# Kernel tuning notes

Measured on AMD Instinct MI355X. Metric: run time of the kernel, lower is better.

## Reference

```python
import jax, jax.numpy as jnp
import numpy as np

B, N, D, H, L, ML, NS = 2, 512, 256, 8, 4, 512, 1000
DH = D // H
DFF = 4 * D

def _layer_norm(x, g, b, eps=1e-5):
    m = jnp.mean(x, -1, keepdims=True)
    v = jnp.var(x, -1, keepdims=True)
    return (x - m) / jnp.sqrt(v + eps) * g + b

def _safe_norm(sq):
    # torch.norm has zero subgradient at 0 (diagonal of pairwise diffs)
    pos = sq > 0
    return jnp.where(pos, jnp.sqrt(jnp.where(pos, sq, 1.0)), 0.0)

def setup_inputs() -> dict:
    key = jax.random.key(0)
    ks = iter(jax.random.split(key, 64))
    w = lambda shape: jax.random.normal(next(ks), shape, jnp.float32) * 0.05
    inp = {
        'x': jax.random.normal(next(ks), (B, N, 3), jnp.float32),
        't': jax.random.randint(next(ks), (B,), 0, NS),
        'mask': jnp.ones((B, N), bool),
        'W_time': w((D, 1)), 'b_time': jnp.zeros((D,), jnp.float32),
        'W_in': w((D, 3 + D)), 'b_in': jnp.zeros((D,), jnp.float32),
        'rel_pos': jax.random.normal(next(ks), (2 * ML - 1, D), jnp.float32),
        'qkv_W': w((L, 3 * D, D)), 'qkv_b': jnp.zeros((L, 3 * D), jnp.float32),
        'ao_W': w((L, D, D)), 'ao_b': jnp.zeros((L, D), jnp.float32),
        'geo_W': w((L, H, 2)), 'geo_b': jnp.zeros((L, H), jnp.float32),
        'pos_W': w((L, H, D)), 'pos_b': jnp.zeros((L, H), jnp.float32),
        'ln1_g': jnp.ones((L, D), jnp.float32), 'ln1_b': jnp.zeros((L, D), jnp.float32),
        'ln2_g': jnp.ones((L, D), jnp.float32), 'ln2_b': jnp.zeros((L, D), jnp.float32),
        'fc1_W': w((L, DFF, D)), 'fc1_b': jnp.zeros((L, DFF), jnp.float32),
        'fc2_W': w((L, D, DFF)), 'fc2_b': jnp.zeros((L, D), jnp.float32),
        'W_out': w((3, D)), 'b_out': jnp.zeros((3,), jnp.float32),
    }
    return inp

def _forward(x, t, mask, W_time, b_time, W_in, b_in, rel_pos, qkv_W, qkv_b, ao_W, ao_b,
             geo_W, geo_b, pos_W, pos_b, ln1_g, ln1_b, ln2_g, ln2_b,
             fc1_W, fc1_b, fc2_W, fc2_b, W_out, b_out):
    tf = (t.astype(jnp.float32) / NS)[:, None]                      # (B,1)
    t_embed = jax.nn.relu(tf @ W_time.T + b_time)[:, None, :]       # (B,1,D)
    t_embed = jnp.broadcast_to(t_embed, (B, N, D))
    h = jax.nn.relu(jnp.concatenate([x, t_embed], -1) @ W_in.T + b_in)  # (B,N,D)

    pos_idx = jnp.arange(N)[:, None] - jnp.arange(N)[None, :] + (ML - 1)
    pe = rel_pos[pos_idx]                                           # (N,N,D)
    mask_j = mask[:, None, None, :]                                 # (B,1,1,N)

    for l in range(L):
        # geometric features: pairwise distance + diag of diff@diff^T (= squared dist)
        diff = h[:, :, None, :] - h[:, None, :, :]                  # (B,N,N,D)
        sq = jnp.sum(diff * diff, -1)                               # (B,N,N)
        geo = jnp.stack([_safe_norm(sq), sq], -1)                   # (B,N,N,2)
        geo_w = jnp.einsum('bijc,hc->bhij', geo, geo_W[l]) + geo_b[l][None, :, None, None]
        pos_w = jnp.einsum('ijd,hd->hij', pe, pos_W[l]) + pos_b[l][:, None, None]

        qkv = (h @ qkv_W[l].T + qkv_b[l]).reshape(B, N, 3, H, DH)
        q, k, v = qkv[:, :, 0], qkv[:, :, 1], qkv[:, :, 2]          # (B,N,H,DH)
        logits = jnp.einsum('bihd,bjhd->bhij', q, k) / np.sqrt(DH)
        logits = logits + geo_w + pos_w[None]
        logits = jnp.where(mask_j, logits, -jnp.inf)
        attn = jax.nn.softmax(logits, -1)
        ao = jnp.einsum('bhij,bjhd->bihd', attn, v).reshape(B, N, D)
        ao = ao @ ao_W[l].T + ao_b[l]

        h = _layer_norm(h + ao, ln1_g[l], ln1_b[l])
        ffn = jax.nn.relu(h @ fc1_W[l].T + fc1_b[l]) @ fc2_W[l].T + fc2_b[l]
        ffn = ffn * mask[:, :, None]
        h = _layer_norm(h + ffn, ln2_g[l], ln2_b[l])

    out = h @ W_out.T + b_out
    return out * mask[:, :, None]

def reference(x, t, mask, W_time, b_time, W_in, b_in, rel_pos, qkv_W, qkv_b, ao_W, ao_b,
              geo_W, geo_b, pos_W, pos_b, ln1_g, ln1_b, ln2_g, ln2_b,
              fc1_W, fc1_b, fc2_W, fc2_b, W_out, b_out):
    return _forward(x, t, mask, W_time, b_time, W_in, b_in, rel_pos, qkv_W, qkv_b,
                    ao_W, ao_b, geo_W, geo_b, pos_W, pos_b, ln1_g, ln1_b, ln2_g, ln2_b,
                    fc1_W, fc1_b, fc2_W, fc2_b, W_out, b_out)
```

## Files before the change

### kernel.cpp

```cpp
#include <hip/hip_runtime.h>
#include <hip/hip_bf16.h>
#include <math.h>


#define B_ 2
#define N_ 512
#define D_ 256
#define H_ 8
#define L_ 4
#define ROWS_ (B_ * N_)

typedef __bf16 bf16;
typedef __bf16 b16x8 __attribute__((ext_vector_type(8)));
typedef __bf16 b16x4 __attribute__((ext_vector_type(4)));
typedef float  f32x4 __attribute__((ext_vector_type(4)));

__global__ void u_kernel(const int* __restrict__ t, const float* __restrict__ W_time,
                         const float* __restrict__ b_time, const float* __restrict__ W_in,
                         const float* __restrict__ b_in, float* __restrict__ u)
{
    int b = blockIdx.x, tid = threadIdx.x;
    __shared__ float te[D_];
    float tf = (float)t[b] / 1000.0f;
    te[tid] = fmaxf(tf * W_time[tid] + b_time[tid], 0.0f);
    __syncthreads();
    float acc = b_in[tid];
    const float* wrow = W_in + (size_t)tid * 259 + 3;
    #pragma unroll 4
    for (int k = 0; k < D_; ++k) acc += wrow[k] * te[k];
    u[b * D_ + tid] = acc;
}

__global__ __launch_bounds__(256) void h0bf_kernel(
    const float* __restrict__ x, const float* __restrict__ W_in,
    const float* __restrict__ u, float* __restrict__ h,
    bf16* __restrict__ hb, float* __restrict__ r2)
{
    int w = threadIdx.x >> 6, lane = threadIdx.x & 63;
    int row = blockIdx.x * 4 + w;
    int b = row >> 9;
    float x0 = x[row * 3 + 0], x1 = x[row * 3 + 1], x2 = x[row * 3 + 2];
    float vv[4];
    #pragma unroll
    for (int e = 0; e < 4; ++e) {
        int d = lane * 4 + e;
        const float* wr = W_in + (size_t)d * 259;
        vv[e] = fmaxf(wr[0] * x0 + wr[1] * x1 + wr[2] * x2 + u[b * D_ + d], 0.0f);
    }
    float4 v = make_float4(vv[0], vv[1], vv[2], vv[3]);
    ((float4*)(h + (size_t)row * D_))[lane] = v;
    b16x4 rb = {(bf16)v.x, (bf16)v.y, (bf16)v.z, (bf16)v.w};
    ((b16x4*)(hb + (size_t)row * D_))[lane] = rb;
    float bx = (float)rb[0], by = (float)rb[1], bz = (float)rb[2], bw = (float)rb[3];
    float q2 = bx * bx + by * by + bz * bz + bw * bw;
    #pragma unroll
    for (int o = 1; o < 64; o <<= 1) q2 += __shfl_xor(q2, o);
    if (lane == 0) r2[row] = q2;
}

__global__ void wcvt_all(const float* __restrict__ qW, const float* __restrict__ aW,
                         const float* __restrict__ f1W, const float* __restrict__ f2W,
                         bf16* __restrict__ dst)
{
    size_t idx = ((size_t)blockIdx.x * 256 + threadIdx.x) * 4;
    int l = (int)(idx / 786432);
    int rem = (int)(idx % 786432);
    const float* src; size_t off;
    if (rem < 196608)      { src = qW  + (size_t)l * 196608; off = rem; }
    else if (rem < 262144) { src = aW  + (size_t)l * 65536;  off = rem - 196608; }
    else if (rem < 524288) { src = f1W + (size_t)l * 262144; off = rem - 262144; }
    else                   { src = f2W + (size_t)l * 262144; off = rem - 524288; }
    float4 v = *(const float4*)(src + off);
    b16x4 r = {(bf16)v.x, (bf16)v.y, (bf16)v.z, (bf16)v.w};
    *(b16x4*)(dst + idx) = r;
}

__global__ void posr_kernel(const float* __restrict__ rel_pos, const float* __restrict__ pos_W,
                            const float* __restrict__ pos_b, float* __restrict__ posr)
{
    int p = blockIdx.x, tid = threadIdx.x;
    __shared__ float pe[D_];
    pe[tid] = rel_pos[(size_t)p * D_ + tid];
    __syncthreads();
    if (tid < L_ * H_) {
        const float* w = pos_W + (size_t)tid * D_;
        float acc = pos_b[tid];
        #pragma unroll 4
        for (int d = 0; d < D_; ++d) acc += pe[d] * w[d];
        posr[(size_t)tid * 1023 + p] = acc;
    }
}

__global__ __launch_bounds__(256) void gemm_bf16(
    const bf16* __restrict__ A, const bf16* __restrict__ W,
    const float* __restrict__ bias, float* __restrict__ Cf, bf16* __restrict__ Cb,
    int M, int Nout, int K, int relu)
{
    __shared__ __align__(16) bf16 As[64 * 64];
    __shared__ __align__(16) bf16 Bs[64 * 64];
    const int tid = threadIdx.x;
    const int bn = blockIdx.x * 64, bm = blockIdx.y * 64;
    const int lane = tid & 63, w = tid >> 6;
    const int wr = w >> 1, wc = w & 1;
    const int r15 = lane & 15, kg = lane >> 4;

    f32x4 acc[2][2] = {};

    const int srow = tid >> 2, q = tid & 3;
    for (int k0 = 0; k0 < K; k0 += 64) {
        const bf16* sa = A + (size_t)(bm + srow) * K + k0 + q * 16;
        b16x8 a0 = *(const b16x8*)sa, a1 = *(const b16x8*)(sa + 8);
        *(b16x8*)&As[srow * 64 + (((2 * q) ^ (srow & 7)) << 3)] = a0;
        *(b16x8*)&As[srow * 64 + (((2 * q + 1) ^ (srow & 7)) << 3)] = a1;
        const bf16* sb = W + (size_t)(bn + srow) * K + k0 + q * 16;
        b16x8 b0 = *(const b16x8*)sb, b1 = *(const b16x8*)(sb + 8);
        *(b16x8*)&Bs[srow * 64 + (((2 * q) ^ (srow & 7)) << 3)] = b0;
        *(b16x8*)&Bs[srow * 64 + (((2 * q + 1) ^ (srow & 7)) << 3)] = b1;
        __syncthreads();

        #pragma unroll
        for (int kt = 0; kt < 2; ++kt) {
            int kc = kt * 4 + kg;
            b16x8 av[2], bv[2];
            #pragma unroll
            for (int f = 0; f < 2; ++f) {
                int ar = wr * 32 + f * 16 + r15;
                av[f] = *(const b16x8*)&As[ar * 64 + ((kc ^ (ar & 7)) << 3)];
                int br = wc * 32 + f * 16 + r15;
                bv[f] = *(const b16x8*)&Bs[br * 64 + ((kc ^ (br & 7)) << 3)];
            }
            acc[0][0] = __builtin_amdgcn_mfma_f32_16x16x32_bf16(av[0], bv[0], acc[0][0], 0, 0, 0);
            acc[0][1] = __builtin_amdgcn_mfma_f32_16x16x32_bf16(av[0], bv[1], acc[0][1], 0, 0, 0);
            acc[1][0] = __builtin_amdgcn_mfma_f32_16x16x32_bf16(av[1], bv[0], acc[1][0], 0, 0, 0);
            acc[1][1] = __builtin_amdgcn_mfma_f32_16x16x32_bf16(av[1], bv[1], acc[1][1], 0, 0, 0);
        }
        __syncthreads();
    }

    const int r4 = lane >> 4;
    #pragma unroll
    for (int fm = 0; fm < 2; ++fm) {
        #pragma unroll
        for (int fn = 0; fn < 2; ++fn) {
            int col = bn + wc * 32 + fn * 16 + r15;
            float bc = bias[col];
            #pragma unroll
            for (int r = 0; r < 4; ++r) {
                int rowi = bm + wr * 32 + fm * 16 + r4 * 4 + r;
                float v = acc[fm][fn][r] + bc;
                if (relu) v = fmaxf(v, 0.0f);
                if (Cb) Cb[(size_t)rowi * Nout + col] = (bf16)v;
                else    Cf[(size_t)rowi * Nout + col] = v;
            }
        }
    }
}

__global__ __launch_bounds__(256) void fatgemm_kernel(
    const bf16* __restrict__ hb, const bf16* __restrict__ Wq,
    const float* __restrict__ qB, bf16* __restrict__ qkd, bf16* __restrict__ vt,
    const float* __restrict__ r2, float* __restrict__ sq)
{
    __shared__ __align__(16) bf16 As[64 * 64];
    __shared__ __align__(16) bf16 Bs[64 * 64];
    const int tid = threadIdx.x;
    const int lane = tid & 63, w = tid >> 6;
    const int wr = w >> 1, wc = w & 1;
    const int r15 = lane & 15, kg = lane >> 4;

    const bool isq = blockIdx.x < 192;
    int bn, bm, gb = 0;
    const bf16 *Ap, *Bp;
    if (isq) {
        bn = (blockIdx.x % 12) * 64; bm = (blockIdx.x / 12) * 64;
        Ap = hb + (size_t)bm * 256;  Bp = Wq + (size_t)bn * 256;
    } else {
        int idx = blockIdx.x - 192;
        gb = idx >> 6;
        int i2 = idx & 63;
        bn = (i2 & 7) * 64;
        bm = (i2 >> 3) * 64;
        Ap = hb + ((size_t)gb * 512 + bm) * 256;
        Bp = hb + ((size_t)gb * 512 + bn) * 256;
    }

    f32x4 acc[2][2] = {};
    const int srow = tid >> 2, q = tid & 3;
    for (int k0 = 0; k0 < 256; k0 += 64) {
        const bf16* sa = Ap + (size_t)srow * 256 + k0 + q * 16;
        b16x8 a0 = *(const b16x8*)sa, a1 = *(const b16x8*)(sa + 8);
        *(b16x8*)&As[srow * 64 + (((2 * q) ^ (srow & 7)) << 3)] = a0;
        *(b16x8*)&As[srow * 64 + (((2 * q + 1) ^ (srow & 7)) << 3)] = a1;
        const bf16* sb = Bp + (size_t)srow * 256 + k0 + q * 16;
        b16x8 b0 = *(const b16x8*)sb, b1 = *(const b16x8*)(sb + 8);
        *(b16x8*)&Bs[srow * 64 + (((2 * q) ^ (srow & 7)) << 3)] = b0;
        *(b16x8*)&Bs[srow * 64 + (((2 * q + 1) ^ (srow & 7)) << 3)] = b1;
        __syncthreads();

        #pragma unroll
        for (int kt = 0; kt < 2; ++kt) {
            int kc = kt * 4 + kg;
            b16x8 av[2], bv[2];
            #pragma unroll
            for (int f = 0; f < 2; ++f) {
                int ar = wr * 32 + f * 16 + r15;
                av[f] = *(const b16x8*)&As[ar * 64 + ((kc ^ (ar & 7)) << 3)];
                int br = wc * 32 + f * 16 + r15;
                bv[f] = *(const b16x8*)&Bs[br * 64 + ((kc ^ (br & 7)) << 3)];
            }
            acc[0][0] = __builtin_amdgcn_mfma_f32_16x16x32_bf16(av[0], bv[0], acc[0][0], 0, 0, 0);
            acc[0][1] = __builtin_amdgcn_mfma_f32_16x16x32_bf16(av[0], bv[1], acc[0][1], 0, 0, 0);
            acc[1][0] = __builtin_amdgcn_mfma_f32_16x16x32_bf16(av[1], bv[0], acc[1][0], 0, 0, 0);
            acc[1][1] = __builtin_amdgcn_mfma_f32_16x16x32_bf16(av[1], bv[1], acc[1][1], 0, 0, 0);
        }
        __syncthreads();
    }

    const int r4 = lane >> 4;
    if (isq) {
        #pragma unroll
        for (int fm = 0; fm < 2; ++fm) {
            #pragma unroll
            for (int fn = 0; fn < 2; ++fn) {
                int col = bn + wc * 32 + fn * 16 + r15;
                float bc = qB[col];
                #pragma unroll
                for (int r = 0; r < 4; ++r) {
                    int rowi = bm + wr * 32 + fm * 16 + r4 * 4 + r;
                    float v = acc[fm][fn][r] + bc;
                    if (col < 512) {
                        qkd[(size_t)rowi * 512 + col] = (bf16)v;
                    } else {
                        int hd = col - 512, hhh = hd >> 5, d = hd & 31;
                        int bb = rowi >> 9, j = rowi & 511;
                        vt[(((size_t)bb * 8 + hhh) * 32 + d) * 512 + j] = (bf16)v;
                    }
                }
            }
        }
    } else {
        const float* r2b = r2 + gb * 512;
        #pragma unroll
        for (int fm = 0; fm < 2; ++fm) {
            #pragma unroll
            for (int fn = 0; fn < 2; ++fn) {
                int j = bn + wc * 32 + fn * 16 + r15;
                float r2j = r2b[j];
                #pragma unroll
                for (int r = 0; r < 4; ++r) {
                    int i = bm + wr * 32 + fm * 16 + r4 * 4 + r;
                    sq[((size_t)gb * 512 + i) * 512 + j] = r2b[i] + r2j - 2.0f * acc[fm][fn][r];
                }
            }
        }
    }
}

__global__ __launch_bounds__(256) void attn_mfma(
    const bf16* __restrict__ qk,
    const bf16* __restrict__ vt,
    const float* __restrict__ sq, const float* __restrict__ posr,
    const float* __restrict__ geoW, const float* __restrict__ geoB,
    bf16* __restrict__ ao)
{
    __shared__ __align__(16) bf16 p_lds[4][2048];
    __shared__ float pos_lds[528];
    __shared__ float olds[4 * 528];
    __shared__ float maxs[4][16];
    __shared__ float sums[4][16];

    const int tid = threadIdx.x;
    const int w = tid >> 6, lane = tid & 63;
    const int qt = blockIdx.x, hh = blockIdx.y, b = blockIdx.z;
    const int q0 = qt * 16;
    const int r15 = lane & 15, kg = lane >> 4;
    const int j0w = w * 128;

    for (int i = tid; i < 527; i += 256) pos_lds[i] = posr[hh * 1023 + q0 + i];
    __syncthreads();

    b16x8 qf = *(const b16x8*)(qk + ((size_t)(b * 512 + q0 + r15)) * 512 + hh * 32 + kg * 8);

    f32x4 zero = {};
    f32x4 st[8];
    #pragma unroll
    for (int jt = 0; jt < 8; ++jt) {
        b16x8 kf = *(const b16x8*)(qk + ((size_t)(b * 512 + j0w + jt * 16 + r15)) * 512
                                      + 256 + hh * 32 + kg * 8);
        st[jt] = __builtin_amdgcn_mfma_f32_16x16x32_bf16(kf, qf, zero, 0, 0, 0);
    }

    const float gw0 = geoW[hh * 2], gw1 = geoW[hh * 2 + 1], gb = geoB[hh];
    const float inv = 0.17677669529663687f;
    const int qq = q0 + r15;
    const float* sqrow = sq + ((size_t)b * 512 + qq) * 512;

    #pragma unroll
    for (int jt = 0; jt < 8; ++jt) {
        int jb = j0w + jt * 16 + kg * 4;
        float4 s4 = *(const float4*)(sqrow + jb);
        #pragma unroll
        for (int r = 0; r < 4; ++r) {
            float sv = (r == 0) ? s4.x : (r == 1) ? s4.y : (r == 2) ? s4.z : s4.w;
            float sn = sv > 0.0f ? sqrtf(sv) : 0.0f;
            st[jt][r] = st[jt][r] * inv + gw0 * sn + gw1 * sv + gb
                      + pos_lds[r15 - (jb + r) + 511];
        }
    }

    float mx = -3e38f;
    #pragma unroll
    for (int jt = 0; jt < 8; ++jt) {
        #pragma unroll
        for (int r = 0; r < 4; ++r) mx = fmaxf(mx, st[jt][r]);
    }
    mx = fmaxf(mx, __shfl_xor(mx, 16));
    mx = fmaxf(mx, __shfl_xor(mx, 32));
    if (lane < 16) maxs[w][r15] = mx;
    __syncthreads();
    float M = fmaxf(fmaxf(maxs[0][r15], maxs[1][r15]), fmaxf(maxs[2][r15], maxs[3][r15]));
    float sm = 0.0f;
    #pragma unroll
    for (int jt = 0; jt < 8; ++jt) {
        #pragma unroll
        for (int r = 0; r < 4; ++r) {
            float e = __expf(st[jt][r] - M);
            st[jt][r] = e; sm += e;
        }
    }
    sm += __shfl_xor(sm, 16);
    sm += __shfl_xor(sm, 32);
    if (lane < 16) sums[w][r15] = sm;

    #pragma unroll
    for (int jt = 0; jt < 8; ++jt) {
        int cc = jt * 2 + (kg >> 1);
        int ccs = cc ^ (r15 & 7);
        b16x4 p4 = {(bf16)st[jt][0], (bf16)st[jt][1], (bf16)st[jt][2], (bf16)st[jt][3]};
        *(b16x4*)&p_lds[w][r15 * 128 + ccs * 8 + (kg & 1) * 4] = p4;
    }

    f32x4 oacc[2] = {};
    #pragma unroll
    for (int jc = 0; jc < 4; ++jc) {
        int ccs = (jc * 4 + kg) ^ (r15 & 7);
        b16x8 pf = *(const b16x8*)&p_lds[w][r15 * 128 + ccs * 8];
        #pragma unroll
        for (int dt = 0; dt < 2; ++dt) {
            b16x8 vf = *(const b16x8*)(vt + (((size_t)(b * 8 + hh)) * 32 + dt * 16 + r15) * 512
                                          + j0w + jc * 32 + kg * 8);
            oacc[dt] = __builtin_amdgcn_mfma_f32_16x16x32_bf16(pf, vf, oacc[dt], 0, 0, 0);
        }
    }
    #pragma unroll
    for (int dt = 0; dt < 2; ++dt) {
        #pragma unroll
        for (int r = 0; r < 4; ++r)
            olds[w * 528 + (kg * 4 + r) * 33 + dt * 16 + r15] = oacc[dt][r];
    }
    __syncthreads();

    #pragma unroll
    for (int it = 0; it < 2; ++it) {
        int idx = tid + it * 256;
        int row = idx >> 5, d = idx & 31;
        float T = sums[0][row] + sums[1][row] + sums[2][row] + sums[3][row];
        float val = olds[row * 33 + d] + olds[528 + row * 33 + d]
                  + olds[1056 + row * 33 + d] + olds[1584 + row * 33 + d];
        ao[((size_t)(b * 512 + q0 + row)) * 256 + hh * 32 + d] = (bf16)(val / T);
    }
}

template <int K>
__global__ __launch_bounds__(256) void gemmln_kernel(
    const bf16* __restrict__ A, const bf16* __restrict__ W,
    const float* __restrict__ bias, float* __restrict__ h,
    const float* __restrict__ g, const float* __restrict__ beta,
    bf16* __restrict__ hb, float* __restrict__ r2out)
{
    __shared__ __align__(16) bf16 As[16 * K];
    __shared__ float reds[3][4][16];
    const int tid = threadIdx.x;
    const int row0 = blockIdx.x * 16;
    const int lane = tid & 63, w = tid >> 6;
    const int r15 = lane & 15, kg = lane >> 4;
    constexpr int NCH = K / 8;
    constexpr int CPT = (16 * NCH) / 256;

    #pragma unroll
    for (int e = 0; e < CPT; ++e) {
        int gch = tid * CPT + e;
        int row = gch / NCH, c = gch % NCH;
        int slab = c >> 3, c3 = c & 7;
        b16x8 v = *(const b16x8*)(A + (size_t)(row0 + row) * K + c * 8);
        *(b16x8*)&As[slab * 1024 + row * 64 + ((c3 ^ (row & 7)) << 3)] = v;
    }
    __syncthreads();

    f32x4 acc[4] = {};
    #pragma unroll 4
    for (int kt = 0; kt < K / 32; ++kt) {
        int slab = kt >> 1, kc2 = (kt & 1) * 4 + kg;
        b16x8 af = *(const b16x8*)&As[slab * 1024 + r15 * 64 + ((kc2 ^ (r15 & 7)) << 3)];
        #pragma unroll
        for (int t = 0; t < 4; ++t) {
            int col = w * 64 + t * 16 + r15;
            b16x8 bf = *(const b16x8*)(W + (size_t)col * K + kt * 32 + kg * 8);
            acc[t] = __builtin_amdgcn_mfma_f32_16x16x32_bf16(af, bf, acc[t], 0, 0, 0);
        }
    }

    float val[4][4];
    #pragma unroll
    for (int t = 0; t < 4; ++t) {
        int col = w * 64 + t * 16 + r15;
        float bc = bias[col];
        #pragma unroll
        for (int r = 0; r < 4; ++r)
            val[t][r] = acc[t][r] + bc + h[(size_t)(row0 + kg * 4 + r) * 256 + col];
    }

    float s[4];
    #pragma unroll
    for (int r = 0; r < 4; ++r) {
        s[r] = val[0][r] + val[1][r] + val[2][r] + val[3][r];
        #pragma unroll
        for (int o = 1; o < 16; o <<= 1) s[r] += __shfl_xor(s[r], o);
    }
    if (r15 == 0) {
        for (int r = 0; r < 4; ++r) reds[0][w][kg * 4 + r] = s[r];
    }
    __syncthreads();
    float mean[4];
    #pragma unroll
    for (int r = 0; r < 4; ++r) {
        int row = kg * 4 + r;
        mean[r] = (reds[0][0][row] + reds[0][1][row] + reds[0][2][row] + reds[0][3][row]) * (1.0f / 256.0f);
    }
    #pragma unroll
    for (int r = 0; r < 4; ++r) {
        float q = 0.0f;
        #pragma unroll
        for (int t = 0; t < 4; ++t) { float d = val[t][r] - mean[r]; q += d * d; }
        #pragma unroll
        for (int o = 1; o < 16; o <<= 1) q += __shfl_xor(q, o);
        s[r] = q;
    }
    __syncthreads();
    if (r15 == 0) {
        for (int r = 0; r < 4; ++r) reds[1][w][kg * 4 + r] = s[r];
    }
    __syncthreads();
    float rstd[4];
    #pragma unroll
    for (int r = 0; r < 4; ++r) {
        int row = kg * 4 + r;
        float var = (reds[1][0][row] + reds[1][1][row] + reds[1][2][row] + reds[1][3][row]) * (1.0f / 256.0f);
        rstd[r] = rsqrtf(var + 1e-5f);
    }
    float q2[4] = {0.f, 0.f, 0.f, 0.f};
    #pragma unroll
    for (int t = 0; t < 4; ++t) {
        int col = w * 64 + t * 16 + r15;
        float gc = g[col], bc2 = beta[col];
        #pragma unroll
        for (int r = 0; r < 4; ++r) {
            int row = row0 + kg * 4 + r;
            float nv = (val[t][r] - mean[r]) * rstd[r] * gc + bc2;
            h[(size_t)row * 256 + col] = nv;
            bf16 nb = (bf16)nv;
            hb[(size_t)row * 256 + col] = nb;
            float f = (float)nb;
            q2[r] += f * f;
        }
    }
    #pragma unroll
    for (int r = 0; r < 4; ++r) {
        #pragma unroll
        for (int o = 1; o < 16; o <<= 1) q2[r] += __shfl_xor(q2[r], o);
    }
    if (r15 == 0) {
        for (int r = 0; r < 4; ++r) reds[2][w][kg * 4 + r] = q2[r];
    }
    __syncthreads();
    if (w == 0 && r15 == 0) {
        for (int r = 0; r < 4; ++r) {
            int row = kg * 4 + r;
            r2out[row0 + row] = reds[2][0][row] + reds[2][1][row] + reds[2][2][row] + reds[2][3][row];
        }
    }
}

__global__ void out_kernel(const float* __restrict__ h, const float* __restrict__ W_out,
                           const float* __restrict__ b_out, float* __restrict__ out)
{
    int idx = blockIdx.x * 256 + threadIdx.x;
    if (idx >= ROWS_ * 3) return;
    int c = idx % 3, row = idx / 3;
    const float* hr = h + (size_t)row * D_;
    const float* w = W_out + (size_t)c * D_;
    float acc = b_out[c];
    #pragma unroll 4
    for (int d = 0; d < D_; ++d) acc += hr[d] * w[d];
    out[idx] = acc;
}

extern "C" void kernel_launch(void* const* d_in, const int* in_sizes, int n_in,
                              void* d_out, int out_size, void* d_ws, size_t ws_size,
                              hipStream_t stream)
{
    const float* x       = (const float*)d_in[0];
    const int*   t       = (const int*)d_in[1];
    const float* W_time  = (const float*)d_in[3];
    const float* b_time  = (const float*)d_in[4];
    const float* W_in    = (const float*)d_in[5];
    const float* b_in    = (const float*)d_in[6];
    const float* rel_pos = (const float*)d_in[7];
    const float* qkv_W   = (const float*)d_in[8];
    const float* qkv_b   = (const float*)d_in[9];
    const float* ao_W    = (const float*)d_in[10];
    const float* ao_b    = (const float*)d_in[11];
    const float* geo_W   = (const float*)d_in[12];
    const float* geo_b   = (const float*)d_in[13];
    const float* pos_W   = (const float*)d_in[14];
    const float* pos_b   = (const float*)d_in[15];
    const float* ln1_g   = (const float*)d_in[16];
    const float* ln1_b   = (const float*)d_in[17];
    const float* ln2_g   = (const float*)d_in[18];
    const float* ln2_b   = (const float*)d_in[19];
    const float* fc1_W   = (const float*)d_in[20];
    const float* fc1_b   = (const float*)d_in[21];
    const float* fc2_W   = (const float*)d_in[22];
    const float* fc2_b   = (const float*)d_in[23];
    const float* W_out   = (const float*)d_in[24];
    const float* b_out   = (const float*)d_in[25];
    float* out = (float*)d_out;

    float* wsf    = (float*)d_ws;
    float* h      = wsf;
    float* sqb    = wsf + 262144;
    float* posr   = wsf + 786432;
    float* uu     = wsf + 819200;
    float* r2     = wsf + 819712;
    bf16*  h_bf   = (bf16*)(wsf + 820736);
    bf16*  ao_bf  = (bf16*)(wsf + 951808);
    bf16*  qk_bf  = (bf16*)(wsf + 1082880);
    bf16*  vt_bf  = (bf16*)(wsf + 1345024);
    bf16*  Wbf    = (bf16*)(wsf + 1476096);
    bf16*  ffn_bf = (bf16*)sqb;

    u_kernel<<<B_, 256, 0, stream>>>(t, W_time, b_time, W_in, b_in, uu);
    h0bf_kernel<<<256, 256, 0, stream>>>(x, W_in, uu, h, h_bf, r2);
    posr_kernel<<<1023, 256, 0, stream>>>(rel_pos, pos_W, pos_b, posr);
    wcvt_all<<<3072, 256, 0, stream>>>(qkv_W, ao_W, fc1_W, fc2_W, Wbf);

    for (int l = 0; l < L_; ++l) {
        bf16* Wl  = Wbf + (size_t)l * 786432;
        bf16* Wq  = Wl;
        bf16* Wao = Wl + 196608;
        bf16* Wf1 = Wl + 262144;
        bf16* Wf2 = Wl + 524288;
        const float* qB  = qkv_b + (size_t)l * 768;
        const float* aB  = ao_b  + (size_t)l * 256;
        const float* gW  = geo_W + (size_t)l * H_ * 2;
        const float* gB  = geo_b + (size_t)l * H_;
        const float* pR  = posr  + (size_t)l * H_ * 1023;
        const float* l1g = ln1_g + (size_t)l * 256;
        const float* l1b = ln1_b + (size_t)l * 256;
        const float* l2g = ln2_g + (size_t)l * 256;
        const float* l2b = ln2_b + (size_t)l * 256;
        const float* f1B = fc1_b + (size_t)l * 1024;
        const float* f2B = fc2_b + (size_t)l * 256;

        fatgemm_kernel<<<320, 256, 0, stream>>>(h_bf, Wq, qB, qk_bf, vt_bf, r2, sqb);
        attn_mfma<<<dim3(32, H_, B_), 256, 0, stream>>>(qk_bf, vt_bf, sqb, pR, gW, gB, ao_bf);
        gemmln_kernel<256><<<64, 256, 0, stream>>>(ao_bf, Wao, aB, h, l1g, l1b, h_bf, r2);
        gemm_bf16<<<dim3(16, 16), 256, 0, stream>>>(h_bf, Wf1, f1B, nullptr, ffn_bf, ROWS_, 1024, 256, 1);
        gemmln_kernel<1024><<<64, 256, 0, stream>>>(ffn_bf, Wf2, f2B, h, l2g, l2b, h_bf, r2);
    }

    out_kernel<<<(ROWS_ * 3 + 255) / 256, 256, 0, stream>>>(h, W_out, b_out, out);
}
```

Before: 267.7 us.

## Merge prep kernels, stage full K=256 tiles in LDS, fuse output projection into last LN

The four setup kernels become one multi-role prep kernel, removing three launches. The FC1 and QKV GEMMs now load the whole 64x256 A and B tiles into shared memory in one step, replacing the four-stage K loop and its per-stage barriers. Shared memory per block grows to 64 KB, which may lower occupancy. The final output projection is folded into the last layernorm GEMM kernel, dropping the separate out kernel.

```diff
diff --git a/kernel.cpp b/kernel.cpp
--- a/kernel.cpp
+++ b/kernel.cpp
@@ -15,126 +15,120 @@
 typedef __bf16 b16x4 __attribute__((ext_vector_type(4)));
 typedef float  f32x4 __attribute__((ext_vector_type(4)));
 
-__global__ void u_kernel(const int* __restrict__ t, const float* __restrict__ W_time,
-                         const float* __restrict__ b_time, const float* __restrict__ W_in,
-                         const float* __restrict__ b_in, float* __restrict__ u)
+__global__ __launch_bounds__(256) void prep_kernel(
+    const float* __restrict__ x, const int* __restrict__ t,
+    const float* __restrict__ W_time, const float* __restrict__ b_time,
+    const float* __restrict__ W_in, const float* __restrict__ b_in,
+    const float* __restrict__ rel_pos, const float* __restrict__ pos_W,
+    const float* __restrict__ pos_b,
+    const float* __restrict__ qW, const float* __restrict__ aW,
+    const float* __restrict__ f1W, const float* __restrict__ f2W,
+    float* __restrict__ h, bf16* __restrict__ hb, float* __restrict__ r2,
+    float* __restrict__ posr, bf16* __restrict__ Wbf)
 {
-    int b = blockIdx.x, tid = threadIdx.x;
-    __shared__ float te[D_];
-    float tf = (float)t[b] / 1000.0f;
-    te[tid] = fmaxf(tf * W_time[tid] + b_time[tid], 0.0f);
-    __syncthreads();
-    float acc = b_in[tid];
-    const float* wrow = W_in + (size_t)tid * 259 + 3;
-    #pragma unroll 4
-    for (int k = 0; k < D_; ++k) acc += wrow[k] * te[k];
-    u[b * D_ + tid] = acc;
+    __shared__ float smem[512];
+    const int tid = threadIdx.x;
+    const int blk = blockIdx.x;
+
+    if (blk < 256) {
+        float* te = smem;
+        float* ul = smem + 256;
+        int row0 = blk * 4;
+        int b = row0 >> 9;
+        float tf = (float)t[b] / 1000.0f;
+        te[tid] = fmaxf(tf * W_time[tid] + b_time[tid], 0.0f);
+        __syncthreads();
+        {
+            float acc = b_in[tid];
+            const float* wrow = W_in + (size_t)tid * 259 + 3;
+            #pragma unroll 4
+            for (int k = 0; k < D_; ++k) acc += wrow[k] * te[k];
+            ul[tid] = acc;
+        }
+        __syncthreads();
+        int w = tid >> 6, lane = tid & 63;
+        int row = row0 + w;
+        float x0 = x[row * 3 + 0], x1 = x[row * 3 + 1], x2 = x[row * 3 + 2];
+        float vv[4];
+        #pragma unroll
+        for (int e = 0; e < 4; ++e) {
+            int d = lane * 4 + e;
+            const float* wr = W_in + (size_t)d * 259;
+            vv[e] = fmaxf(wr[0] * x0 + wr[1] * x1 + wr[2] * x2 + ul[d], 0.0f);
+        }
+        float4 v = make_float4(vv[0], vv[1], vv[2], vv[3]);
+        ((float4*)(h + (size_t)row * D_))[lane] = v;
+        b16x4 rb = {(bf16)v.x, (bf16)v.y, (bf16)v.z, (bf16)v.w};
+        ((b16x4*)(hb + (size_t)row * D_))[lane] = rb;
+        float bx = (float)rb[0], by = (float)rb[1], bz = (float)rb[2], bw = (float)rb[3];
+        float q2 = bx * bx + by * by + bz * bz + bw * bw;
+        #pragma unroll
+        for (int o = 1; o < 64; o <<= 1) q2 += __shfl_xor(q2, o);
+        if (lane == 0) r2[row] = q2;
+    } else if (blk < 1279) {
+        int p = blk - 256;
+        float* pe = smem;
+        pe[tid] = rel_pos[(size_t)p * D_ + tid];
+        __syncthreads();
+        if (tid < L_ * H_) {
+            const float* w = pos_W + (size_t)tid * D_;
+            float acc = pos_b[tid];
+            #pragma unroll 4
+            for (int d = 0; d < D_; ++d) acc += pe[d] * w[d];
+            posr[(size_t)tid * 1023 + p] = acc;
+        }
+    } else {
+        size_t idx = ((size_t)(blk - 1279) * 256 + tid) * 4;
+        int l = (int)(idx / 786432);
+        int rem = (int)(idx % 786432);
+        const float* src; size_t off;
+        if (rem < 196608)      { src = qW  + (size_t)l * 196608; off = rem; }
+        else if (rem < 262144) { src = aW  + (size_t)l * 65536;  off = rem - 196608; }
+        else if (rem < 524288) { src = f1W + (size_t)l * 262144; off = rem - 262144; }
+        else                   { src = f2W + (size_t)l * 262144; off = rem - 524288; }
+        float4 v = *(const float4*)(src + off);
+        b16x4 r = {(bf16)v.x, (bf16)v.y, (bf16)v.z, (bf16)v.w};
+        *(b16x4*)(Wbf + idx) = r;
+    }
 }
 
-__global__ __launch_bounds__(256) void h0bf_kernel(
-    const float* __restrict__ x, const float* __restrict__ W_in,
-    const float* __restrict__ u, float* __restrict__ h,
-    bf16* __restrict__ hb, float* __restrict__ r2)
+__global__ __launch_bounds__(256) void gemm_k256(
+    const bf16* __restrict__ A, const bf16* __restrict__ W,
+    const float* __restrict__ bias, bf16* __restrict__ Cb, int Nout, int relu)
 {
-    int w = threadIdx.x >> 6, lane = threadIdx.x & 63;
-    int row = blockIdx.x * 4 + w;
-    int b = row >> 9;
-    float x0 = x[row * 3 + 0], x1 = x[row * 3 + 1], x2 = x[row * 3 + 2];
-    float vv[4];
-    #pragma unroll
-    for (int e = 0; e < 4; ++e) {
-        int d = lane * 4 + e;
-        const float* wr = W_in + (size_t)d * 259;
-        vv[e] = fmaxf(wr[0] * x0 + wr[1] * x1 + wr[2] * x2 + u[b * D_ + d], 0.0f);
-    }
-    float4 v = make_float4(vv[0], vv[1], vv[2], vv[3]);
-    ((float4*)(h + (size_t)row * D_))[lane] = v;
-    b16x4 rb = {(bf16)v.x, (bf16)v.y, (bf16)v.z, (bf16)v.w};
-    ((b16x4*)(hb + (size_t)row * D_))[lane] = rb;
-    float bx = (float)rb[0], by = (float)rb[1], bz = (float)rb[2], bw = (float)rb[3];
-    float q2 = bx * bx + by * by + bz * bz + bw * bw;
-    #pragma unroll
-    for (int o = 1; o < 64; o <<= 1) q2 += __shfl_xor(q2, o);
-    if (lane == 0) r2[row] = q2;
-}
-
-__global__ void wcvt_all(const float* __restrict__ qW, const float* __restrict__ aW,
-                         const float* __restrict__ f1W, const float* __restrict__ f2W,
-                         bf16* __restrict__ dst)
-{
-    size_t idx = ((size_t)blockIdx.x * 256 + threadIdx.x) * 4;
-    int l = (int)(idx / 786432);
-    int rem = (int)(idx % 786432);
-    const float* src; size_t off;
-    if (rem < 196608)      { src = qW  + (size_t)l * 196608; off = rem; }
-    else if (rem < 262144) { src = aW  + (size_t)l * 65536;  off = rem - 196608; }
-    else if (rem < 524288) { src = f1W + (size_t)l * 262144; off = rem - 262144; }
-    else                   { src = f2W + (size_t)l * 262144; off = rem - 524288; }
-    float4 v = *(const float4*)(src + off);
-    b16x4 r = {(bf16)v.x, (bf16)v.y, (bf16)v.z, (bf16)v.w};
-    *(b16x4*)(dst + idx) = r;
-}
-
-__global__ void posr_kernel(const float* __restrict__ rel_pos, const float* __restrict__ pos_W,
-                            const float* __restrict__ pos_b, float* __restrict__ posr)
-{
-    int p = blockIdx.x, tid = threadIdx.x;
-    __shared__ float pe[D_];
-    pe[tid] = rel_pos[(size_t)p * D_ + tid];
-    __syncthreads();
-    if (tid < L_ * H_) {
-        const float* w = pos_W + (size_t)tid * D_;
-        float acc = pos_b[tid];
-        #pragma unroll 4
-        for (int d = 0; d < D_; ++d) acc += pe[d] * w[d];
-        posr[(size_t)tid * 1023 + p] = acc;
-    }
-}
-
-__global__ __launch_bounds__(256) void gemm_bf16(
-    const bf16* __restrict__ A, const bf16* __restrict__ W,
-    const float* __restrict__ bias, float* __restrict__ Cf, bf16* __restrict__ Cb,
-    int M, int Nout, int K, int relu)
-{
-    __shared__ __align__(16) bf16 As[64 * 64];
-    __shared__ __align__(16) bf16 Bs[64 * 64];
+    __shared__ __align__(16) bf16 As[64 * 256];
+    __shared__ __align__(16) bf16 Bs[64 * 256];
     const int tid = threadIdx.x;
     const int bn = blockIdx.x * 64, bm = blockIdx.y * 64;
     const int lane = tid & 63, w = tid >> 6;
     const int wr = w >> 1, wc = w & 1;
     const int r15 = lane & 15, kg = lane >> 4;
 
+    #pragma unroll
+    for (int i = 0; i < 8; ++i) {
+        int g = tid + 256 * i;
+        int row = g >> 5, c = g & 31, cs = c ^ (row & 7);
+        *(b16x8*)&As[row * 256 + cs * 8] = *(const b16x8*)(A + (size_t)(bm + row) * 256 + c * 8);
+        *(b16x8*)&Bs[row * 256 + cs * 8] = *(const b16x8*)(W + (size_t)(bn + row) * 256 + c * 8);
+    }
+    __syncthreads();
+
     f32x4 acc[2][2] = {};
-
-    const int srow = tid >> 2, q = tid & 3;
-    for (int k0 = 0; k0 < K; k0 += 64) {
-        const bf16* sa = A + (size_t)(bm + srow) * K + k0 + q * 16;
-        b16x8 a0 = *(const b16x8*)sa, a1 = *(const b16x8*)(sa + 8);
-        *(b16x8*)&As[srow * 64 + (((2 * q) ^ (srow & 7)) << 3)] = a0;
-        *(b16x8*)&As[srow * 64 + (((2 * q + 1) ^ (srow & 7)) << 3)] = a1;
-        const bf16* sb = W + (size_t)(bn + srow) * K + k0 + q * 16;
-        b16x8 b0 = *(const b16x8*)sb, b1 = *(const b16x8*)(sb + 8);
-        *(b16x8*)&Bs[srow * 64 + (((2 * q) ^ (srow & 7)) << 3)] = b0;
-        *(b16x8*)&Bs[srow * 64 + (((2 * q + 1) ^ (srow & 7)) << 3)] = b1;
-        __syncthreads();
-
-        #pragma unroll
-        for (int kt = 0; kt < 2; ++kt) {
-            int kc = kt * 4 + kg;
-            b16x8 av[2], bv[2];
-            #pragma unroll
-            for (int f = 0; f < 2; ++f) {
-                int ar = wr * 32 + f * 16 + r15;
-                av[f] = *(const b16x8*)&As[ar * 64 + ((kc ^ (ar & 7)) << 3)];
-                int br = wc * 32 + f * 16 + r15;
-                bv[f] = *(const b16x8*)&Bs[br * 64 + ((kc ^ (br & 7)) << 3)];
-            }
-            acc[0][0] = __builtin_amdgcn_mfma_f32_16x16x32_bf16(av[0], bv[0], acc[0][0], 0, 0, 0);
-            acc[0][1] = __builtin_amdgcn_mfma_f32_16x16x32_bf16(av[0], bv[1], acc[0][1], 0, 0, 0);
-            acc[1][0] = __builtin_amdgcn_mfma_f32_16x16x32_bf16(av[1], bv[0], acc[1][0], 0, 0, 0);
-            acc[1][1] = __builtin_amdgcn_mfma_f32_16x16x32_bf16(av[1], bv[1], acc[1][1], 0, 0, 0);
-        }
-        __syncthreads();
+    #pragma unroll
+    for (int st = 0; st < 8; ++st) {
+        int c0 = st * 4 + kg;
+        b16x8 av[2], bv[2];
+        #pragma unroll
+        for (int f = 0; f < 2; ++f) {
+            int ar = wr * 32 + f * 16 + r15;
+            av[f] = *(const b16x8*)&As[ar * 256 + ((c0 ^ (ar & 7)) << 3)];
+            int br = wc * 32 + f * 16 + r15;
+            bv[f] = *(const b16x8*)&Bs[br * 256 + ((c0 ^ (br & 7)) << 3)];
+        }
+        acc[0][0] = __builtin_amdgcn_mfma_f32_16x16x32_bf16(av[0], bv[0], acc[0][0], 0, 0, 0);
+        acc[0][1] = __builtin_amdgcn_mfma_f32_16x16x32_bf16(av[0], bv[1], acc[0][1], 0, 0, 0);
+        acc[1][0] = __builtin_amdgcn_mfma_f32_16x16x32_bf16(av[1], bv[0], acc[1][0], 0, 0, 0);
+        acc[1][1] = __builtin_amdgcn_mfma_f32_16x16x32_bf16(av[1], bv[1], acc[1][1], 0, 0, 0);
     }
 
     const int r4 = lane >> 4;
@@ -149,8 +143,7 @@
                 int rowi = bm + wr * 32 + fm * 16 + r4 * 4 + r;
                 float v = acc[fm][fn][r] + bc;
                 if (relu) v = fmaxf(v, 0.0f);
-                if (Cb) Cb[(size_t)rowi * Nout + col] = (bf16)v;
-                else    Cf[(size_t)rowi * Nout + col] = v;
+                Cb[(size_t)rowi * Nout + col] = (bf16)v;
             }
         }
     }
@@ -161,8 +154,8 @@
     const float* __restrict__ qB, bf16* __restrict__ qkd, bf16* __restrict__ vt,
     const float* __restrict__ r2, float* __restrict__ sq)
 {
-    __shared__ __align__(16) bf16 As[64 * 64];
-    __shared__ __align__(16) bf16 Bs[64 * 64];
+    __shared__ __align__(16) bf16 As[64 * 256];
+    __shared__ __align__(16) bf16 Bs[64 * 256];
     const int tid = threadIdx.x;
     const int lane = tid & 63, w = tid >> 6;
     const int wr = w >> 1, wc = w & 1;
@@ -184,36 +177,31 @@
         Bp = hb + ((size_t)gb * 512 + bn) * 256;
     }
 
+    #pragma unroll
+    for (int i = 0; i < 8; ++i) {
+        int g = tid + 256 * i;
+        int row = g >> 5, c = g & 31, cs = c ^ (row & 7);
+        *(b16x8*)&As[row * 256 + cs * 8] = *(const b16x8*)(Ap + (size_t)row * 256 + c * 8);
+        *(b16x8*)&Bs[row * 256 + cs * 8] = *(const b16x8*)(Bp + (size_t)row * 256 + c * 8);
+    }
+    __syncthreads();
+
     f32x4 acc[2][2] = {};
-    const int srow = tid >> 2, q = tid & 3;
-    for (int k0 = 0; k0 < 256; k0 += 64) {
-        const bf16* sa = Ap + (size_t)srow * 256 + k0 + q * 16;
-        b16x8 a0 = *(const b16x8*)sa, a1 = *(const b16x8*)(sa + 8);
-        *(b16x8*)&As[srow * 64 + (((2 * q) ^ (srow & 7)) << 3)] = a0;
-        *(b16x8*)&As[srow * 64 + (((2 * q + 1) ^ (srow & 7)) << 3)] = a1;
-        const bf16* sb = Bp + (size_t)srow * 256 + k0 + q * 16;
-        b16x8 b0 = *(const b16x8*)sb, b1 = *(const b16x8*)(sb + 8);
-        *(b16x8*)&Bs[srow * 64 + (((2 * q) ^ (srow & 7)) << 3)] = b0;
-        *(b16x8*)&Bs[srow * 64 + (((2 * q + 1) ^ (srow & 7)) << 3)] = b1;
-        __syncthreads();
-
-        #pragma unroll
-        for (int kt = 0; kt < 2; ++kt) {
-            int kc = kt * 4 + kg;
-            b16x8 av[2], bv[2];
-            #pragma unroll
-            for (int f = 0; f < 2; ++f) {
-                int ar = wr * 32 + f * 16 + r15;
-                av[f] = *(const b16x8*)&As[ar * 64 + ((kc ^ (ar & 7)) << 3)];
-                int br = wc * 32 + f * 16 + r15;
-                bv[f] = *(const b16x8*)&Bs[br * 64 + ((kc ^ (br & 7)) << 3)];
-            }
-            acc[0][0] = __builtin_amdgcn_mfma_f32_16x16x32_bf16(av[0], bv[0], acc[0][0], 0, 0, 0);
-            acc[0][1] = __builtin_amdgcn_mfma_f32_16x16x32_bf16(av[0], bv[1], acc[0][1], 0, 0, 0);
-            acc[1][0] = __builtin_amdgcn_mfma_f32_16x16x32_bf16(av[1], bv[0], acc[1][0], 0, 0, 0);
-            acc[1][1] = __builtin_amdgcn_mfma_f32_16x16x32_bf16(av[1], bv[1], acc[1][1], 0, 0, 0);
-        }
-        __syncthreads();
+    #pragma unroll
+    for (int st = 0; st < 8; ++st) {
+        int c0 = st * 4 + kg;
+        b16x8 av[2], bv[2];
+        #pragma unroll
+        for (int f = 0; f < 2; ++f) {
+            int ar = wr * 32 + f * 16 + r15;
+            av[f] = *(const b16x8*)&As[ar * 256 + ((c0 ^ (ar & 7)) << 3)];
+            int br = wc * 32 + f * 16 + r15;
+            bv[f] = *(const b16x8*)&Bs[br * 256 + ((c0 ^ (br & 7)) << 3)];
+        }
+        acc[0][0] = __builtin_amdgcn_mfma_f32_16x16x32_bf16(av[0], bv[0], acc[0][0], 0, 0, 0);
+        acc[0][1] = __builtin_amdgcn_mfma_f32_16x16x32_bf16(av[0], bv[1], acc[0][1], 0, 0, 0);
+        acc[1][0] = __builtin_amdgcn_mfma_f32_16x16x32_bf16(av[1], bv[0], acc[1][0], 0, 0, 0);
+        acc[1][1] = __builtin_amdgcn_mfma_f32_16x16x32_bf16(av[1], bv[1], acc[1][1], 0, 0, 0);
     }
 
     const int r4 = lane >> 4;
@@ -257,8 +245,7 @@
 }
 
 __global__ __launch_bounds__(256) void attn_mfma(
-    const bf16* __restrict__ qk,
-    const bf16* __restrict__ vt,
+    const bf16* __restrict__ qk, const bf16* __restrict__ vt,
     const float* __restrict__ sq, const float* __restrict__ posr,
     const float* __restrict__ geoW, const float* __restrict__ geoB,
     bf16* __restrict__ ao)
@@ -376,7 +363,9 @@
     const bf16* __restrict__ A, const bf16* __restrict__ W,
     const float* __restrict__ bias, float* __restrict__ h,
     const float* __restrict__ g, const float* __restrict__ beta,
-    bf16* __restrict__ hb, float* __restrict__ r2out)
+    bf16* __restrict__ hb, float* __restrict__ r2out,
+    const float* __restrict__ Wout, const float* __restrict__ bout,
+    float* __restrict__ outp)
 {
     __shared__ __align__(16) bf16 As[16 * K];
     __shared__ float reds[3][4][16];
@@ -459,6 +448,7 @@
         rstd[r] = rsqrtf(var + 1e-5f);
     }
     float q2[4] = {0.f, 0.f, 0.f, 0.f};
+    float nvv[4][4];
     #pragma unroll
     for (int t = 0; t < 4; ++t) {
         int col = w * 64 + t * 16 + r15;
@@ -467,6 +457,7 @@
         for (int r = 0; r < 4; ++r) {
             int row = row0 + kg * 4 + r;
             float nv = (val[t][r] - mean[r]) * rstd[r] * gc + bc2;
+            nvv[t][r] = nv;
             h[(size_t)row * 256 + col] = nv;
             bf16 nb = (bf16)nv;
             hb[(size_t)row * 256 + col] = nb;
@@ -489,20 +480,46 @@
             r2out[row0 + row] = reds[2][0][row] + reds[2][1][row] + reds[2][2][row] + reds[2][3][row];
         }
     }
-}
-
-__global__ void out_kernel(const float* __restrict__ h, const float* __restrict__ W_out,
-                           const float* __restrict__ b_out, float* __restrict__ out)
-{
-    int idx = blockIdx.x * 256 + threadIdx.x;
-    if (idx >= ROWS_ * 3) return;
-    int c = idx % 3, row = idx / 3;
-    const float* hr = h + (size_t)row * D_;
-    const float* w = W_out + (size_t)c * D_;
-    float acc = b_out[c];
-    #pragma unroll 4
-    for (int d = 0; d < D_; ++d) acc += hr[d] * w[d];
-    out[idx] = acc;
+
+    if (Wout) {
+        float oc[3][4];
+        #pragma unroll
+        for (int c = 0; c < 3; ++c) {
+            #pragma unroll
+            for (int r = 0; r < 4; ++r) oc[c][r] = 0.0f;
+        }
+        #pragma unroll
+        for (int t = 0; t < 4; ++t) {
+            int col = w * 64 + t * 16 + r15;
+            float w0 = Wout[0 * 256 + col], w1 = Wout[1 * 256 + col], w2 = Wout[2 * 256 + col];
+            #pragma unroll
+            for (int r = 0; r < 4; ++r) {
+                oc[0][r] += nvv[t][r] * w0;
+                oc[1][r] += nvv[t][r] * w1;
+                oc[2][r] += nvv[t][r] * w2;
+            }
+        }
+        #pragma unroll
+        for (int c = 0; c < 3; ++c) {
+            #pragma unroll
+            for (int r = 0; r < 4; ++r) {
+                #pragma unroll
+                for (int o = 1; o < 16; o <<= 1) oc[c][r] += __shfl_xor(oc[c][r], o);
+            }
+        }
+        __syncthreads();
+        if (r15 == 0) {
+            for (int c = 0; c < 3; ++c) {
+                for (int r = 0; r < 4; ++r) reds[c][w][kg * 4 + r] = oc[c][r];
+            }
+        }
+        __syncthreads();
+        if (tid < 48) {
+            int c = tid / 16, row = tid % 16;
+            float v = reds[c][0][row] + reds[c][1][row] + reds[c][2][row] + reds[c][3][row] + bout[c];
+            outp[(size_t)(row0 + row) * 3 + c] = v;
+        }
+    }
 }
 
 extern "C" void kernel_launch(void* const* d_in, const int* in_sizes, int n_in,
@@ -540,7 +557,6 @@
     float* h      = wsf;
     float* sqb    = wsf + 262144;
     float* posr   = wsf + 786432;
-    float* uu     = wsf + 819200;
     float* r2     = wsf + 819712;
     bf16*  h_bf   = (bf16*)(wsf + 820736);
     bf16*  ao_bf  = (bf16*)(wsf + 951808);
@@ -549,10 +565,10 @@
     bf16*  Wbf    = (bf16*)(wsf + 1476096);
     bf16*  ffn_bf = (bf16*)sqb;
 
-    u_kernel<<<B_, 256, 0, stream>>>(t, W_time, b_time, W_in, b_in, uu);
-    h0bf_kernel<<<256, 256, 0, stream>>>(x, W_in, uu, h, h_bf, r2);
-    posr_kernel<<<1023, 256, 0, stream>>>(rel_pos, pos_W, pos_b, posr);
-    wcvt_all<<<3072, 256, 0, stream>>>(qkv_W, ao_W, fc1_W, fc2_W, Wbf);
+    prep_kernel<<<4351, 256, 0, stream>>>(x, t, W_time, b_time, W_in, b_in,
+                                          rel_pos, pos_W, pos_b,
+                                          qkv_W, ao_W, fc1_W, fc2_W,
+                                          h, h_bf, r2, posr, Wbf);
 
     for (int l = 0; l < L_; ++l) {
         bf16* Wl  = Wbf + (size_t)l * 786432;
@@ -571,13 +587,16 @@
         const float* l2b = ln2_b + (size_t)l * 256;
         const float* f1B = fc1_b + (size_t)l * 1024;
         const float* f2B = fc2_b + (size_t)l * 256;
+        const bool last = (l == L_ - 1);
 
         fatgemm_kernel<<<320, 256, 0, stream>>>(h_bf, Wq, qB, qk_bf, vt_bf, r2, sqb);
         attn_mfma<<<dim3(32, H_, B_), 256, 0, stream>>>(qk_bf, vt_bf, sqb, pR, gW, gB, ao_bf);
-        gemmln_kernel<256><<<64, 256, 0, stream>>>(ao_bf, Wao, aB, h, l1g, l1b, h_bf, r2);
-        gemm_bf16<<<dim3(16, 16), 256, 0, stream>>>(h_bf, Wf1, f1B, nullptr, ffn_bf, ROWS_, 1024, 256, 1);
-        gemmln_kernel<1024><<<64, 256, 0, stream>>>(ffn_bf, Wf2, f2B, h, l2g, l2b, h_bf, r2);
-    }
-
-    out_kernel<<<(ROWS_ * 3 + 255) / 256, 256, 0, stream>>>(h, W_out, b_out, out);
+        gemmln_kernel<256><<<64, 256, 0, stream>>>(ao_bf, Wao, aB, h, l1g, l1b, h_bf, r2,
+                                                   nullptr, nullptr, nullptr);
+        gemm_k256<<<dim3(16, 16), 256, 0, stream>>>(h_bf, Wf1, f1B, ffn_bf, 1024, 1);
+        gemmln_kernel<1024><<<64, 256, 0, stream>>>(ffn_bf, Wf2, f2B, h, l2g, l2b, h_bf, r2,
+                                                    last ? W_out : nullptr,
+                                                    last ? b_out : nullptr,
+                                                    last ? out : nullptr);
+    }
 }
```

New measurement: 238.7 us. -10.8%, faster.
